# Optimization experiments

Measured on AMD Instinct MI355X. Metric: run time of the kernel, lower is better.

The kernel has to match this reference:

```python
import jax, jax.numpy as jnp
import numpy as np

B, L, H, NH, NB = 8, 200, 128, 4, 2
HD = H // NH
ITEM_NUM, TIME_SPAN = 50000, 256
PAD = -2.0**32 + 1.0


def setup_inputs() -> dict:
    key = jax.random.key(0)
    ks = jax.random.split(key, 32)
    def g(i, shape, s=0.02):
        return jax.random.normal(ks[i], shape, jnp.float32) * s
    item_emb = g(0, (ITEM_NUM + 1, H)).at[0].set(0.0)  # padding_idx=0
    return dict(
        user_ids=jax.random.randint(ks[1], (B,), 0, 1000),
        log_seqs=jax.random.randint(ks[2], (B, L), 0, ITEM_NUM),
        time_matrices=jax.random.randint(ks[3], (B, L, L), 0, TIME_SPAN + 1),
        pos_seqs=jax.random.randint(ks[4], (B, L), 0, ITEM_NUM + 1),
        neg_seqs=jax.random.randint(ks[5], (B, L), 0, ITEM_NUM + 1),
        item_emb=item_emb,
        pos_K_emb=g(6, (L, H)), pos_V_emb=g(7, (L, H)),
        time_K_emb=g(8, (TIME_SPAN + 1, H)), time_V_emb=g(9, (TIME_SPAN + 1, H)),
        attn_ln_g=jnp.ones((NB, H)), attn_ln_b=jnp.zeros((NB, H)),
        Wq=g(10, (NB, H, H)), bq=jnp.zeros((NB, H)),
        Wk=g(11, (NB, H, H)), bk=jnp.zeros((NB, H)),
        Wv=g(12, (NB, H, H)), bv=jnp.zeros((NB, H)),
        fwd_ln_g=jnp.ones((NB, H)), fwd_ln_b=jnp.zeros((NB, H)),
        W1=g(13, (NB, H, H)), b1=jnp.zeros((NB, H)),
        W2=g(14, (NB, H, H)), b2=jnp.zeros((NB, H)),
        last_ln_g=jnp.ones((H,)), last_ln_b=jnp.zeros((H,)),
    )


def _ln(x, g, b, eps=1e-8):
    m = x.mean(-1, keepdims=True)
    v = jnp.var(x, axis=-1, keepdims=True)
    return (x - m) / jnp.sqrt(v + eps) * g + b


def _heads(x):
    # [..., H] -> [NH, ..., HD]; matches torch.cat(torch.split(x, HD, -1), 0)
    y = x.reshape(x.shape[:-1] + (NH, HD))
    return jnp.moveaxis(y, -2, 0)


def reference(user_ids, log_seqs, time_matrices, pos_seqs, neg_seqs, item_emb,
              pos_K_emb, pos_V_emb, time_K_emb, time_V_emb,
              attn_ln_g, attn_ln_b, Wq, bq, Wk, bk, Wv, bv,
              fwd_ln_g, fwd_ln_b, W1, b1, W2, b2, last_ln_g, last_ln_b):
    # user_ids is unused in the original forward as well.
    tmask = log_seqs == 0                                  # [B,L] True = pad
    keep = (~tmask)[..., None].astype(jnp.float32)
    seqs = item_emb[log_seqs] * np.float32(np.sqrt(H))
    seqs = seqs * keep
    pKh = _heads(pos_K_emb)                                # [NH,L,HD]
    pVh = _heads(pos_V_emb)
    tKh = _heads(time_K_emb[time_matrices])                # [NH,B,L,L,HD]
    tVh = _heads(time_V_emb[time_matrices])
    causal = ~jnp.tril(jnp.ones((L, L), bool))             # True above diag -> masked
    bad = tmask[:, :, None] | causal[None]                 # [B,L,L]
    scale = np.float32(np.sqrt(HD))
    for i in range(NB):
        Qin = _ln(seqs, attn_ln_g[i], attn_ln_b[i])
        Qh = _heads(Qin @ Wq[i].T + bq[i])                 # [NH,B,L,HD]
        Kh = _heads(seqs @ Wk[i].T + bk[i])
        Vh = _heads(seqs @ Wv[i].T + bv[i])
        attn = (jnp.einsum('nbqd,nbkd->nbqk', Qh, Kh)
                + jnp.einsum('nbqd,nkd->nbqk', Qh, pKh)
                + jnp.einsum('nbqkd,nbqd->nbqk', tKh, Qh)) / scale
        attn = jnp.where(bad[None], PAD, attn)
        attn = jax.nn.softmax(attn, axis=-1)
        out = (jnp.einsum('nbqk,nbkd->nbqd', attn, Vh)
               + jnp.einsum('nbqk,nkd->nbqd', attn, pVh)
               + jnp.einsum('nbqk,nbqkd->nbqd', attn, tVh))
        out = jnp.moveaxis(out, 0, -2).reshape(seqs.shape)  # merge heads -> [B,L,H]
        seqs = Qin + out                                    # residual uses LN'd Q (as in source)
        seqs = _ln(seqs, fwd_ln_g[i], fwd_ln_b[i])
        ff = jax.nn.relu(seqs @ W1[i].T + b1[i]) @ W2[i].T + b2[i] + seqs
        seqs = ff * keep
    log_feats = _ln(seqs, last_ln_g, last_ln_b)
    pos_logits = (log_feats * item_emb[pos_seqs]).sum(-1)   # [B,L]
    neg_logits = (log_feats * item_emb[neg_seqs]).sum(-1)
    return pos_logits, neg_logits
```

## Files before the change

kernel.cpp:

```cpp
#include <hip/hip_runtime.h>

#define BB 8
#define LL 200
#define HH 128
#define NHEAD 4
#define HDIM 32
#define NBLK 2
#define BL (BB * LL)
#define NT 257
#define QT 8
#define NQT 25
#define SSP 208
#define KTP 66
#define TSP 132

static constexpr float SQRT_H    = 11.313708498984761f;
static constexpr float INV_SCALE = 0.17677669529663687f;
static constexpr float PADV      = -4294967295.0f;

__global__ void k_qkv_gemm(const float* __restrict__ seqs_in,
                           const int* __restrict__ log_seqs,
                           const float* __restrict__ item_emb,
                           const float* __restrict__ g, const float* __restrict__ bia,
                           const float* __restrict__ Wq, const float* __restrict__ bq,
                           const float* __restrict__ Wk, const float* __restrict__ bk,
                           const float* __restrict__ Wv, const float* __restrict__ bv,
                           const float* __restrict__ posK, const float* __restrict__ posV,
                           float* __restrict__ Qin, float* __restrict__ Q,
                           float* __restrict__ K, float* __restrict__ V) {
    int mt = blockIdx.x / 24, nt = blockIdx.x % 24;
    int matsel = nt >> 3;
    int jb = (nt & 7) * 16;
    int row0 = mt * 32;
    int tid = threadIdx.x;
    __shared__ float As[32 * TSP];
    __shared__ float Bs[16 * TSP];

    {
        int r = tid >> 3, seg = tid & 7;
        int row = row0 + r;
        float4 vv[4];
        if (seqs_in) {
            #pragma unroll
            for (int i = 0; i < 4; i++)
                vv[i] = *(const float4*)(seqs_in + (size_t)row * HH + seg * 16 + i * 4);
        } else {
            int idx = log_seqs[row];
            if (idx == 0) {
                #pragma unroll
                for (int i = 0; i < 4; i++) vv[i] = make_float4(0.f, 0.f, 0.f, 0.f);
            } else {
                #pragma unroll
                for (int i = 0; i < 4; i++) {
                    float4 e = *(const float4*)(item_emb + (size_t)idx * HH + seg * 16 + i * 4);
                    vv[i] = make_float4(e.x * SQRT_H, e.y * SQRT_H, e.z * SQRT_H, e.w * SQRT_H);
                }
            }
        }
        if (matsel == 0) {
            float s = 0.f, s2 = 0.f;
            #pragma unroll
            for (int i = 0; i < 4; i++) {
                s  += vv[i].x + vv[i].y + vv[i].z + vv[i].w;
                s2 += vv[i].x * vv[i].x + vv[i].y * vv[i].y + vv[i].z * vv[i].z + vv[i].w * vv[i].w;
            }
            #pragma unroll
            for (int off = 1; off < 8; off <<= 1) {
                s  += __shfl_xor(s, off);
                s2 += __shfl_xor(s2, off);
            }
            float mean = s * (1.f / HH);
            float var  = s2 * (1.f / HH) - mean * mean;
            float inv  = 1.f / sqrtf(var + 1e-8f);
            #pragma unroll
            for (int i = 0; i < 4; i++) {
                int k = seg * 16 + i * 4;
                float4 g4 = *(const float4*)(g + k);
                float4 b4 = *(const float4*)(bia + k);
                float4 y;
                y.x = (vv[i].x - mean) * inv * g4.x + b4.x;
                y.y = (vv[i].y - mean) * inv * g4.y + b4.y;
                y.z = (vv[i].z - mean) * inv * g4.z + b4.z;
                y.w = (vv[i].w - mean) * inv * g4.w + b4.w;
                *(float4*)&As[r * TSP + k] = y;
                if (nt == 0) *(float4*)(Qin + (size_t)row * HH + k) = y;
            }
        } else {
            #pragma unroll
            for (int i = 0; i < 4; i++)
                *(float4*)&As[r * TSP + seg * 16 + i * 4] = vv[i];
        }
    }
    {
        const float* W = (matsel == 0) ? Wq : (matsel == 1) ? Wk : Wv;
        int j = tid >> 4, seg = tid & 15;
        *(float4*)&Bs[j * TSP + seg * 8]     = *(const float4*)(W + (size_t)(jb + j) * HH + seg * 8);
        *(float4*)&Bs[j * TSP + seg * 8 + 4] = *(const float4*)(W + (size_t)(jb + j) * HH + seg * 8 + 4);
    }
    __syncthreads();

    int m = tid >> 3, jg = tid & 7;
    float acc0 = 0.f, acc1 = 0.f;
    const float* ar = &As[m * TSP];
    const float* b0r = &Bs[(jg * 2) * TSP];
    const float* b1r = &Bs[(jg * 2 + 1) * TSP];
    #pragma unroll 4
    for (int k4 = 0; k4 < 32; k4++) {
        float4 a = *(const float4*)(ar + k4 * 4);
        float4 b0 = *(const float4*)(b0r + k4 * 4);
        float4 b1 = *(const float4*)(b1r + k4 * 4);
        acc0 += a.x * b0.x + a.y * b0.y + a.z * b0.z + a.w * b0.w;
        acc1 += a.x * b1.x + a.y * b1.y + a.z * b1.z + a.w * b1.w;
    }
    int row = row0 + m;
    int col = jb + jg * 2;
    int l = row % LL;
    if (matsel == 0) {
        float2 bb = *(const float2*)(bq + col);
        *(float2*)(Q + (size_t)row * HH + col) =
            make_float2((acc0 + bb.x) * INV_SCALE, (acc1 + bb.y) * INV_SCALE);
    } else if (matsel == 1) {
        float2 bb = *(const float2*)(bk + col);
        float2 pk = *(const float2*)(posK + (size_t)l * HH + col);
        *(float2*)(K + (size_t)row * HH + col) =
            make_float2(acc0 + bb.x + pk.x, acc1 + bb.y + pk.y);
    } else {
        float2 bb = *(const float2*)(bv + col);
        float2 pv = *(const float2*)(posV + (size_t)l * HH + col);
        *(float2*)(V + (size_t)row * HH + col) =
            make_float2(acc0 + bb.x + pv.x, acc1 + bb.y + pv.y);
    }
}

__global__ void k_attn(const float* __restrict__ Q, const float* __restrict__ K,
                       const float* __restrict__ V,
                       const float* __restrict__ timeK, const float* __restrict__ timeV,
                       const int* __restrict__ tm,
                       float* __restrict__ att) {
    int bn = blockIdx.x & 31;
    int b = bn >> 2, n = bn & 3;
    int qt = (NQT - 1) - (blockIdx.x >> 5);
    int q0 = qt * QT;
    int kmax = q0 + QT - 1;
    int tid = threadIdx.x;
    int wv = tid >> 6, ln = tid & 63;

    __shared__ float Qs[QT * HDIM];
    __shared__ float KstT[2][HDIM * KTP];
    __shared__ float DTW[QT * NT];
    __shared__ float Ssc[QT * SSP];
    __shared__ unsigned short tmst[QT * LL];
    __shared__ float Ost[QT * HDIM];

    int nchS = (kmax >> 6) + 1;
    int ntot = 5 + nchS;

    auto stage = [&](int c, int buf) {
        const float* src;
        int base, lim;
        if (c < 5) { base = c * 64; src = timeK; lim = NT; }
        else       { base = (c - 5) * 64; src = K + ((size_t)(b * LL)) * HH; lim = LL; }
        #pragma unroll
        for (int pp = 0; pp < 2; pp++) {
            int idx = tid + pp * 256;
            int r = idx >> 3, d4 = idx & 7;
            int rr = base + r;
            float4 w = make_float4(0.f, 0.f, 0.f, 0.f);
            if (rr < lim) w = *(const float4*)(src + (size_t)rr * HH + n * HDIM + d4 * 4);
            KstT[buf][(d4 * 4 + 0) * KTP + r] = w.x;
            KstT[buf][(d4 * 4 + 1) * KTP + r] = w.y;
            KstT[buf][(d4 * 4 + 2) * KTP + r] = w.z;
            KstT[buf][(d4 * 4 + 3) * KTP + r] = w.w;
        }
    };

    Ost[tid] = 0.f;
    if (tid < 64) {
        int qi = tid >> 3, d4 = tid & 7;
        *(float4*)(Qs + qi * HDIM + d4 * 4) =
            *(const float4*)(Q + ((size_t)(b * LL + q0 + qi)) * HH + n * HDIM + d4 * 4);
    }
    #pragma unroll
    for (int qi = 0; qi < QT; qi++)
        if (tid < LL)
            tmst[qi * LL + tid] = (unsigned short)tm[((size_t)(b * LL + q0 + qi)) * LL + tid];
    stage(0, 0);
    __syncthreads();

    int k2 = tid & 31, qi_c = tid >> 5;

    for (int c = 0; c < ntot; c++) {
        int buf = c & 1;
        if (c + 1 < ntot) stage(c + 1, buf ^ 1);
        float a0 = 0.f, a1 = 0.f;
        #pragma unroll 4
        for (int d = 0; d < HDIM; d++) {
            float qv = Qs[qi_c * HDIM + d];
            float2 kv = *(const float2*)&KstT[buf][d * KTP + k2 * 2];
            a0 += qv * kv.x; a1 += qv * kv.y;
        }
        if (c < 5) {
            int tau0 = c * 64 + k2 * 2;
            if (tau0 < NT)     DTW[qi_c * NT + tau0]     = a0;
            if (tau0 + 1 < NT) DTW[qi_c * NT + tau0 + 1] = a1;
        } else {
            int q = q0 + qi_c;
            int k0 = (c - 5) * 64 + k2 * 2;
            if (k0 <= kmax)
                Ssc[qi_c * SSP + k0] = (k0 <= q) ? (a0 + DTW[qi_c * NT + tmst[qi_c * LL + k0]]) : PADV;
            if (k0 + 1 <= kmax)
                Ssc[qi_c * SSP + k0 + 1] = (k0 + 1 <= q) ? (a1 + DTW[qi_c * NT + tmst[qi_c * LL + k0 + 1]]) : PADV;
        }
        __syncthreads();
    }

    for (int idx = tid; idx < QT * NT; idx += 256) DTW[idx] = 0.f;
    __syncthreads();

    for (int rr = 0; rr < 2; rr++) {
        int qi = wv + rr * 4;
        int q = q0 + qi;
        float sv[4];
        float m = PADV;
        #pragma unroll
        for (int jj = 0; jj < 4; jj++) {
            int k = ln + 64 * jj;
            sv[jj] = (k <= q) ? Ssc[qi * SSP + k] : PADV;
            m = fmaxf(m, sv[jj]);
        }
        for (int off = 32; off; off >>= 1) m = fmaxf(m, __shfl_xor(m, off));
        float sum = 0.f;
        #pragma unroll
        for (int jj = 0; jj < 4; jj++) {
            int k = ln + 64 * jj;
            sv[jj] = (k <= q) ? __expf(sv[jj] - m) : 0.f;
            sum += sv[jj];
        }
        for (int off = 32; off; off >>= 1) sum += __shfl_xor(sum, off);
        float inv = 1.f / sum;
        #pragma unroll
        for (int jj = 0; jj < 4; jj++) {
            int k = ln + 64 * jj;
            float pr = sv[jj] * inv;
            if (k < SSP) Ssc[qi * SSP + k] = (k <= q) ? pr : 0.f;
            if (k <= q) atomicAdd(&DTW[qi * NT + tmst[qi * LL + k]], pr);
        }
    }
    __syncthreads();

    int d = tid & 31, kg = tid >> 5;
    float acc[QT] = {0,0,0,0,0,0,0,0};
    const float* vb = V + ((size_t)(b * LL)) * HH + n * HDIM + d;
    for (int k = kg; k <= kmax; k += 8) {
        float v = vb[(size_t)k * HH];
        #pragma unroll
        for (int qi = 0; qi < QT; qi++) acc[qi] += Ssc[qi * SSP + k] * v;
    }
    const float* tvb = timeV + n * HDIM + d;
    for (int t = kg; t < NT; t += 8) {
        float v = tvb[(size_t)t * HH];
        #pragma unroll
        for (int qi = 0; qi < QT; qi++) acc[qi] += DTW[qi * NT + t] * v;
    }
    #pragma unroll
    for (int qi = 0; qi < QT; qi++) atomicAdd(&Ost[qi * HDIM + d], acc[qi]);
    __syncthreads();
    {
        int qi = tid >> 5;
        att[((size_t)(b * LL + q0 + qi)) * HH + n * HDIM + (tid & 31)] = Ost[tid];
    }
}

__global__ void k_ff1(const float* __restrict__ Qin, const float* __restrict__ att,
                      const float* __restrict__ g, const float* __restrict__ bia,
                      const float* __restrict__ W1, const float* __restrict__ b1,
                      float* __restrict__ h1) {
    int mt = blockIdx.x >> 3, jb = (blockIdx.x & 7) * 16;
    int row0 = mt * 16;
    int tid = threadIdx.x;
    __shared__ float As[16 * TSP];
    __shared__ float Bs[16 * TSP];

    {
        int r = tid >> 4, seg = tid & 15;
        int row = row0 + r;
        float4 vv[2];
        #pragma unroll
        for (int i = 0; i < 2; i++) {
            int k = seg * 8 + i * 4;
            float4 q4 = *(const float4*)(Qin + (size_t)row * HH + k);
            float4 a4 = *(const float4*)(att + (size_t)row * HH + k);
            vv[i] = make_float4(q4.x + a4.x, q4.y + a4.y, q4.z + a4.z, q4.w + a4.w);
        }
        float s = 0.f, s2 = 0.f;
        #pragma unroll
        for (int i = 0; i < 2; i++) {
            s  += vv[i].x + vv[i].y + vv[i].z + vv[i].w;
            s2 += vv[i].x * vv[i].x + vv[i].y * vv[i].y + vv[i].z * vv[i].z + vv[i].w * vv[i].w;
        }
        #pragma unroll
        for (int off = 1; off < 16; off <<= 1) {
            s  += __shfl_xor(s, off);
            s2 += __shfl_xor(s2, off);
        }
        float mean = s * (1.f / HH);
        float var  = s2 * (1.f / HH) - mean * mean;
        float inv  = 1.f / sqrtf(var + 1e-8f);
        #pragma unroll
        for (int i = 0; i < 2; i++) {
            int k = seg * 8 + i * 4;
            float4 g4 = *(const float4*)(g + k);
            float4 b4 = *(const float4*)(bia + k);
            float4 y;
            y.x = (vv[i].x - mean) * inv * g4.x + b4.x;
            y.y = (vv[i].y - mean) * inv * g4.y + b4.y;
            y.z = (vv[i].z - mean) * inv * g4.z + b4.z;
            y.w = (vv[i].w - mean) * inv * g4.w + b4.w;
            *(float4*)&As[r * TSP + k] = y;
        }
    }
    {
        int j = tid >> 4, seg = tid & 15;
        *(float4*)&Bs[j * TSP + seg * 8]     = *(const float4*)(W1 + (size_t)(jb + j) * HH + seg * 8);
        *(float4*)&Bs[j * TSP + seg * 8 + 4] = *(const float4*)(W1 + (size_t)(jb + j) * HH + seg * 8 + 4);
    }
    __syncthreads();

    int m = tid >> 4, j = tid & 15;
    float acc = 0.f;
    const float* ar = &As[m * TSP];
    const float* br = &Bs[j * TSP];
    #pragma unroll 4
    for (int k4 = 0; k4 < 32; k4++) {
        float4 a = *(const float4*)(ar + k4 * 4);
        float4 b = *(const float4*)(br + k4 * 4);
        acc += a.x * b.x + a.y * b.y + a.z * b.z + a.w * b.w;
    }
    int col = jb + j;
    float t = acc + b1[col];
    h1[(size_t)(row0 + m) * HH + col] = t > 0.f ? t : 0.f;
}

__global__ void k_ff2(const float* __restrict__ h1,
                      const float* __restrict__ Qin, const float* __restrict__ att,
                      const float* __restrict__ g, const float* __restrict__ bia,
                      const float* __restrict__ W2, const float* __restrict__ b2,
                      const int* __restrict__ log_seqs,
                      float* __restrict__ out) {
    int mt = blockIdx.x >> 3, jb = (blockIdx.x & 7) * 16;
    int row0 = mt * 16;
    int tid = threadIdx.x;
    __shared__ float As[16 * TSP];
    __shared__ float Bs[16 * TSP];
    __shared__ float mu[16], rstd[16];

    {
        int r = tid >> 4, seg = tid & 15;
        int row = row0 + r;
        #pragma unroll
        for (int i = 0; i < 2; i++) {
            int k = seg * 8 + i * 4;
            *(float4*)&As[r * TSP + k] = *(const float4*)(h1 + (size_t)row * HH + k);
        }
        float s = 0.f, s2 = 0.f;
        #pragma unroll
        for (int i = 0; i < 2; i++) {
            int k = seg * 8 + i * 4;
            float4 q4 = *(const float4*)(Qin + (size_t)row * HH + k);
            float4 a4 = *(const float4*)(att + (size_t)row * HH + k);
            float4 v = make_float4(q4.x + a4.x, q4.y + a4.y, q4.z + a4.z, q4.w + a4.w);
            s  += v.x + v.y + v.z + v.w;
            s2 += v.x * v.x + v.y * v.y + v.z * v.z + v.w * v.w;
        }
        #pragma unroll
        for (int off = 1; off < 16; off <<= 1) {
            s  += __shfl_xor(s, off);
            s2 += __shfl_xor(s2, off);
        }
        float mean = s * (1.f / HH);
        float var  = s2 * (1.f / HH) - mean * mean;
        if (seg == 0) { mu[r] = mean; rstd[r] = 1.f / sqrtf(var + 1e-8f); }
    }
    {
        int j = tid >> 4, seg = tid & 15;
        *(float4*)&Bs[j * TSP + seg * 8]     = *(const float4*)(W2 + (size_t)(jb + j) * HH + seg * 8);
        *(float4*)&Bs[j * TSP + seg * 8 + 4] = *(const float4*)(W2 + (size_t)(jb + j) * HH + seg * 8 + 4);
    }
    __syncthreads();

    int m = tid >> 4, j = tid & 15;
    float acc = 0.f;
    const float* ar = &As[m * TSP];
    const float* br = &Bs[j * TSP];
    #pragma unroll 4
    for (int k4 = 0; k4 < 32; k4++) {
        float4 a = *(const float4*)(ar + k4 * 4);
        float4 b = *(const float4*)(br + k4 * 4);
        acc += a.x * b.x + a.y * b.y + a.z * b.z + a.w * b.w;
    }
    int row = row0 + m;
    int col = jb + j;
    float resid = Qin[(size_t)row * HH + col] + att[(size_t)row * HH + col];
    float y = (resid - mu[m]) * rstd[m] * g[col] + bia[col];
    float o = acc + b2[col] + y;
    if (log_seqs[row] == 0) o = 0.f;
    out[(size_t)row * HH + col] = o;
}

__global__ void k_lnlogits(const float* __restrict__ seqs,
                           const float* __restrict__ g, const float* __restrict__ bia,
                           const float* __restrict__ item_emb,
                           const int* __restrict__ pos, const int* __restrict__ neg,
                           float* __restrict__ out) {
    int row = blockIdx.x;
    int h = threadIdx.x;
    float v = seqs[(size_t)row * HH + h];
    float s = v, s2 = v * v;
    for (int off = 32; off; off >>= 1) {
        s  += __shfl_xor(s, off);
        s2 += __shfl_xor(s2, off);
    }
    __shared__ float r1[2], r2[2];
    if ((h & 63) == 0) { r1[h >> 6] = s; r2[h >> 6] = s2; }
    __syncthreads();
    float mean = (r1[0] + r1[1]) * (1.f / HH);
    float var  = (r2[0] + r2[1]) * (1.f / HH) - mean * mean;
    float inv = 1.f / sqrtf(var + 1e-8f);
    float f = (v - mean) * inv * g[h] + bia[h];

    int ip = pos[row], in_ = neg[row];
    float vp = f * item_emb[(size_t)ip * HH + h];
    float vn = f * item_emb[(size_t)in_ * HH + h];
    for (int off = 32; off; off >>= 1) {
        vp += __shfl_xor(vp, off);
        vn += __shfl_xor(vn, off);
    }
    __shared__ float rp[2], rn[2];
    if ((h & 63) == 0) { rp[h >> 6] = vp; rn[h >> 6] = vn; }
    __syncthreads();
    if (h == 0) {
        out[row]      = rp[0] + rp[1];
        out[BL + row] = rn[0] + rn[1];
    }
}

extern "C" void kernel_launch(void* const* d_in, const int* in_sizes, int n_in,
                              void* d_out, int out_size, void* d_ws, size_t ws_size,
                              hipStream_t stream) {
    const int* log_seqs   = (const int*)d_in[1];
    const int* tm         = (const int*)d_in[2];
    const int* pos_seqs   = (const int*)d_in[3];
    const int* neg_seqs   = (const int*)d_in[4];
    const float* item_emb = (const float*)d_in[5];
    const float* posK     = (const float*)d_in[6];
    const float* posV     = (const float*)d_in[7];
    const float* timeK    = (const float*)d_in[8];
    const float* timeV    = (const float*)d_in[9];
    const float* attn_g   = (const float*)d_in[10];
    const float* attn_b   = (const float*)d_in[11];
    const float* Wq       = (const float*)d_in[12];
    const float* bq       = (const float*)d_in[13];
    const float* Wk       = (const float*)d_in[14];
    const float* bk       = (const float*)d_in[15];
    const float* Wv       = (const float*)d_in[16];
    const float* bv       = (const float*)d_in[17];
    const float* fwd_g    = (const float*)d_in[18];
    const float* fwd_b    = (const float*)d_in[19];
    const float* W1       = (const float*)d_in[20];
    const float* b1       = (const float*)d_in[21];
    const float* W2       = (const float*)d_in[22];
    const float* b2       = (const float*)d_in[23];
    const float* last_g   = (const float*)d_in[24];
    const float* last_b   = (const float*)d_in[25];

    float* seqs = (float*)d_ws;
    float* Qin  = seqs + (size_t)BL * HH;
    float* Qb   = Qin  + (size_t)BL * HH;
    float* Kb   = Qb   + (size_t)BL * HH;
    float* Vb   = Kb   + (size_t)BL * HH;
    float* att  = Vb   + (size_t)BL * HH;
    float* h1   = att  + (size_t)BL * HH;

    for (int i = 0; i < NBLK; i++) {
        k_qkv_gemm<<<1200, 256, 0, stream>>>(i == 0 ? nullptr : seqs, log_seqs, item_emb,
                                             attn_g + i * HH, attn_b + i * HH,
                                             Wq + (size_t)i * HH * HH, bq + i * HH,
                                             Wk + (size_t)i * HH * HH, bk + i * HH,
                                             Wv + (size_t)i * HH * HH, bv + i * HH,
                                             posK, posV, Qin, Qb, Kb, Vb);
        k_attn<<<NQT * 32, 256, 0, stream>>>(Qb, Kb, Vb, timeK, timeV, tm, att);
        k_ff1<<<800, 256, 0, stream>>>(Qin, att, fwd_g + i * HH, fwd_b + i * HH,
                                       W1 + (size_t)i * HH * HH, b1 + i * HH, h1);
        k_ff2<<<800, 256, 0, stream>>>(h1, Qin, att, fwd_g + i * HH, fwd_b + i * HH,
                                       W2 + (size_t)i * HH * HH, b2 + i * HH,
                                       log_seqs, seqs);
    }
    k_lnlogits<<<BL, HH, 0, stream>>>(seqs, last_g, last_b, item_emb,
                                      pos_seqs, neg_seqs, (float*)d_out);
}
```

Baseline: 239.8 us.

## Fuse FFN layers and final LayerNorm logits into one kernel; cache Q in registers

The two feed-forward GEMM kernels and the final LayerNorm-plus-logits kernel become a single kernel. Each block handles 4 rows and keeps the LN output and the hidden activations in shared memory, so the h1 round trip through global memory and two launches per block go away. In the attention kernel the Q row is loaded into registers once, instead of being re-read from shared memory in every chunk. The trade-off is that each block now reloads both full 128x128 weight matrices into shared memory for only 4 rows, which adds weight traffic and leaves little compute per block to hide it.

```diff
diff --git a/kernel.cpp b/kernel.cpp
--- a/kernel.cpp
+++ b/kernel.cpp
@@ -13,6 +13,8 @@
 #define SSP 208
 #define KTP 66
 #define TSP 132
+#define BSP 66
+#define FSP 132
 
 static constexpr float SQRT_H    = 11.313708498984761f;
 static constexpr float INV_SCALE = 0.17677669529663687f;
@@ -189,15 +191,18 @@
 
     int k2 = tid & 31, qi_c = tid >> 5;
 
+    float qreg[HDIM];
+    #pragma unroll
+    for (int d = 0; d < HDIM; d++) qreg[d] = Qs[qi_c * HDIM + d];
+
     for (int c = 0; c < ntot; c++) {
         int buf = c & 1;
         if (c + 1 < ntot) stage(c + 1, buf ^ 1);
         float a0 = 0.f, a1 = 0.f;
-        #pragma unroll 4
+        #pragma unroll 8
         for (int d = 0; d < HDIM; d++) {
-            float qv = Qs[qi_c * HDIM + d];
             float2 kv = *(const float2*)&KstT[buf][d * KTP + k2 * 2];
-            a0 += qv * kv.x; a1 += qv * kv.y;
+            a0 += qreg[d] * kv.x; a1 += qreg[d] * kv.y;
         }
         if (c < 5) {
             int tau0 = c * 64 + k2 * 2;
@@ -271,176 +276,111 @@
     }
 }
 
-__global__ void k_ff1(const float* __restrict__ Qin, const float* __restrict__ att,
+__global__ void k_ffn(const float* __restrict__ Qin, const float* __restrict__ att,
                       const float* __restrict__ g, const float* __restrict__ bia,
                       const float* __restrict__ W1, const float* __restrict__ b1,
-                      float* __restrict__ h1) {
-    int mt = blockIdx.x >> 3, jb = (blockIdx.x & 7) * 16;
-    int row0 = mt * 16;
+                      const float* __restrict__ W2, const float* __restrict__ b2,
+                      const int* __restrict__ log_seqs,
+                      const float* __restrict__ lg, const float* __restrict__ lb,
+                      const float* __restrict__ item_emb,
+                      const int* __restrict__ pos, const int* __restrict__ neg,
+                      float* __restrict__ out, float* __restrict__ logits, int last) {
+    int row0 = blockIdx.x * 4;
     int tid = threadIdx.x;
-    __shared__ float As[16 * TSP];
-    __shared__ float Bs[16 * TSP];
+    int wv = tid >> 6, ln = tid & 63;
+    __shared__ float As[4 * FSP];
+    __shared__ float H1[4 * FSP];
+    __shared__ float Bs[128 * BSP];
 
     {
-        int r = tid >> 4, seg = tid & 15;
-        int row = row0 + r;
-        float4 vv[2];
-        #pragma unroll
-        for (int i = 0; i < 2; i++) {
-            int k = seg * 8 + i * 4;
-            float4 q4 = *(const float4*)(Qin + (size_t)row * HH + k);
-            float4 a4 = *(const float4*)(att + (size_t)row * HH + k);
-            vv[i] = make_float4(q4.x + a4.x, q4.y + a4.y, q4.z + a4.z, q4.w + a4.w);
-        }
-        float s = 0.f, s2 = 0.f;
-        #pragma unroll
-        for (int i = 0; i < 2; i++) {
-            s  += vv[i].x + vv[i].y + vv[i].z + vv[i].w;
-            s2 += vv[i].x * vv[i].x + vv[i].y * vv[i].y + vv[i].z * vv[i].z + vv[i].w * vv[i].w;
-        }
-        #pragma unroll
-        for (int off = 1; off < 16; off <<= 1) {
+        int row = row0 + wv;
+        float v0 = Qin[(size_t)row * HH + ln]      + att[(size_t)row * HH + ln];
+        float v1 = Qin[(size_t)row * HH + ln + 64] + att[(size_t)row * HH + ln + 64];
+        float s = v0 + v1, s2 = v0 * v0 + v1 * v1;
+        for (int off = 32; off; off >>= 1) {
             s  += __shfl_xor(s, off);
             s2 += __shfl_xor(s2, off);
         }
         float mean = s * (1.f / HH);
         float var  = s2 * (1.f / HH) - mean * mean;
         float inv  = 1.f / sqrtf(var + 1e-8f);
-        #pragma unroll
-        for (int i = 0; i < 2; i++) {
-            int k = seg * 8 + i * 4;
-            float4 g4 = *(const float4*)(g + k);
-            float4 b4 = *(const float4*)(bia + k);
-            float4 y;
-            y.x = (vv[i].x - mean) * inv * g4.x + b4.x;
-            y.y = (vv[i].y - mean) * inv * g4.y + b4.y;
-            y.z = (vv[i].z - mean) * inv * g4.z + b4.z;
-            y.w = (vv[i].w - mean) * inv * g4.w + b4.w;
-            *(float4*)&As[r * TSP + k] = y;
-        }
-    }
-    {
-        int j = tid >> 4, seg = tid & 15;
-        *(float4*)&Bs[j * TSP + seg * 8]     = *(const float4*)(W1 + (size_t)(jb + j) * HH + seg * 8);
-        *(float4*)&Bs[j * TSP + seg * 8 + 4] = *(const float4*)(W1 + (size_t)(jb + j) * HH + seg * 8 + 4);
-    }
-    __syncthreads();
-
-    int m = tid >> 4, j = tid & 15;
-    float acc = 0.f;
-    const float* ar = &As[m * TSP];
-    const float* br = &Bs[j * TSP];
-    #pragma unroll 4
-    for (int k4 = 0; k4 < 32; k4++) {
-        float4 a = *(const float4*)(ar + k4 * 4);
-        float4 b = *(const float4*)(br + k4 * 4);
-        acc += a.x * b.x + a.y * b.y + a.z * b.z + a.w * b.w;
-    }
-    int col = jb + j;
-    float t = acc + b1[col];
-    h1[(size_t)(row0 + m) * HH + col] = t > 0.f ? t : 0.f;
-}
-
-__global__ void k_ff2(const float* __restrict__ h1,
-                      const float* __restrict__ Qin, const float* __restrict__ att,
-                      const float* __restrict__ g, const float* __restrict__ bia,
-                      const float* __restrict__ W2, const float* __restrict__ b2,
-                      const int* __restrict__ log_seqs,
-                      float* __restrict__ out) {
-    int mt = blockIdx.x >> 3, jb = (blockIdx.x & 7) * 16;
-    int row0 = mt * 16;
-    int tid = threadIdx.x;
-    __shared__ float As[16 * TSP];
-    __shared__ float Bs[16 * TSP];
-    __shared__ float mu[16], rstd[16];
-
-    {
-        int r = tid >> 4, seg = tid & 15;
-        int row = row0 + r;
-        #pragma unroll
-        for (int i = 0; i < 2; i++) {
-            int k = seg * 8 + i * 4;
-            *(float4*)&As[r * TSP + k] = *(const float4*)(h1 + (size_t)row * HH + k);
-        }
-        float s = 0.f, s2 = 0.f;
-        #pragma unroll
-        for (int i = 0; i < 2; i++) {
-            int k = seg * 8 + i * 4;
-            float4 q4 = *(const float4*)(Qin + (size_t)row * HH + k);
-            float4 a4 = *(const float4*)(att + (size_t)row * HH + k);
-            float4 v = make_float4(q4.x + a4.x, q4.y + a4.y, q4.z + a4.z, q4.w + a4.w);
-            s  += v.x + v.y + v.z + v.w;
-            s2 += v.x * v.x + v.y * v.y + v.z * v.z + v.w * v.w;
-        }
-        #pragma unroll
-        for (int off = 1; off < 16; off <<= 1) {
+        As[wv * FSP + ln]      = (v0 - mean) * inv * g[ln]      + bia[ln];
+        As[wv * FSP + ln + 64] = (v1 - mean) * inv * g[ln + 64] + bia[ln + 64];
+    }
+    __syncthreads();
+
+    int jx = ln;
+    for (int c = 0; c < 2; c++) {
+        int k4 = tid & 31, jj0 = tid >> 5;
+        #pragma unroll
+        for (int p = 0; p < 8; p++) {
+            int jj = jj0 + p * 8;
+            float4 w = *(const float4*)(W1 + (size_t)(c * 64 + jj) * HH + k4 * 4);
+            Bs[(k4 * 4 + 0) * BSP + jj] = w.x;
+            Bs[(k4 * 4 + 1) * BSP + jj] = w.y;
+            Bs[(k4 * 4 + 2) * BSP + jj] = w.z;
+            Bs[(k4 * 4 + 3) * BSP + jj] = w.w;
+        }
+        __syncthreads();
+        float acc = 0.f;
+        #pragma unroll 8
+        for (int k = 0; k < HH; k++)
+            acc += As[wv * FSP + k] * Bs[k * BSP + jx];
+        int col = c * 64 + jx;
+        float t = acc + b1[col];
+        H1[wv * FSP + col] = t > 0.f ? t : 0.f;
+        __syncthreads();
+    }
+
+    int rowm = row0 + wv;
+    int keepz = (log_seqs[rowm] == 0);
+    for (int c = 0; c < 2; c++) {
+        int k4 = tid & 31, jj0 = tid >> 5;
+        #pragma unroll
+        for (int p = 0; p < 8; p++) {
+            int jj = jj0 + p * 8;
+            float4 w = *(const float4*)(W2 + (size_t)(c * 64 + jj) * HH + k4 * 4);
+            Bs[(k4 * 4 + 0) * BSP + jj] = w.x;
+            Bs[(k4 * 4 + 1) * BSP + jj] = w.y;
+            Bs[(k4 * 4 + 2) * BSP + jj] = w.z;
+            Bs[(k4 * 4 + 3) * BSP + jj] = w.w;
+        }
+        __syncthreads();
+        float acc = 0.f;
+        #pragma unroll 8
+        for (int k = 0; k < HH; k++)
+            acc += H1[wv * FSP + k] * Bs[k * BSP + jx];
+        int col = c * 64 + jx;
+        float o = acc + b2[col] + As[wv * FSP + col];
+        if (keepz) o = 0.f;
+        if (!last) out[(size_t)rowm * HH + col] = o;
+        As[wv * FSP + col] = o;
+        __syncthreads();
+    }
+
+    if (last) {
+        float o0 = As[wv * FSP + ln], o1 = As[wv * FSP + ln + 64];
+        float s = o0 + o1, s2 = o0 * o0 + o1 * o1;
+        for (int off = 32; off; off >>= 1) {
             s  += __shfl_xor(s, off);
             s2 += __shfl_xor(s2, off);
         }
         float mean = s * (1.f / HH);
         float var  = s2 * (1.f / HH) - mean * mean;
-        if (seg == 0) { mu[r] = mean; rstd[r] = 1.f / sqrtf(var + 1e-8f); }
-    }
-    {
-        int j = tid >> 4, seg = tid & 15;
-        *(float4*)&Bs[j * TSP + seg * 8]     = *(const float4*)(W2 + (size_t)(jb + j) * HH + seg * 8);
-        *(float4*)&Bs[j * TSP + seg * 8 + 4] = *(const float4*)(W2 + (size_t)(jb + j) * HH + seg * 8 + 4);
-    }
-    __syncthreads();
-
-    int m = tid >> 4, j = tid & 15;
-    float acc = 0.f;
-    const float* ar = &As[m * TSP];
-    const float* br = &Bs[j * TSP];
-    #pragma unroll 4
-    for (int k4 = 0; k4 < 32; k4++) {
-        float4 a = *(const float4*)(ar + k4 * 4);
-        float4 b = *(const float4*)(br + k4 * 4);
-        acc += a.x * b.x + a.y * b.y + a.z * b.z + a.w * b.w;
-    }
-    int row = row0 + m;
-    int col = jb + j;
-    float resid = Qin[(size_t)row * HH + col] + att[(size_t)row * HH + col];
-    float y = (resid - mu[m]) * rstd[m] * g[col] + bia[col];
-    float o = acc + b2[col] + y;
-    if (log_seqs[row] == 0) o = 0.f;
-    out[(size_t)row * HH + col] = o;
-}
-
-__global__ void k_lnlogits(const float* __restrict__ seqs,
-                           const float* __restrict__ g, const float* __restrict__ bia,
-                           const float* __restrict__ item_emb,
-                           const int* __restrict__ pos, const int* __restrict__ neg,
-                           float* __restrict__ out) {
-    int row = blockIdx.x;
-    int h = threadIdx.x;
-    float v = seqs[(size_t)row * HH + h];
-    float s = v, s2 = v * v;
-    for (int off = 32; off; off >>= 1) {
-        s  += __shfl_xor(s, off);
-        s2 += __shfl_xor(s2, off);
-    }
-    __shared__ float r1[2], r2[2];
-    if ((h & 63) == 0) { r1[h >> 6] = s; r2[h >> 6] = s2; }
-    __syncthreads();
-    float mean = (r1[0] + r1[1]) * (1.f / HH);
-    float var  = (r2[0] + r2[1]) * (1.f / HH) - mean * mean;
-    float inv = 1.f / sqrtf(var + 1e-8f);
-    float f = (v - mean) * inv * g[h] + bia[h];
-
-    int ip = pos[row], in_ = neg[row];
-    float vp = f * item_emb[(size_t)ip * HH + h];
-    float vn = f * item_emb[(size_t)in_ * HH + h];
-    for (int off = 32; off; off >>= 1) {
-        vp += __shfl_xor(vp, off);
-        vn += __shfl_xor(vn, off);
-    }
-    __shared__ float rp[2], rn[2];
-    if ((h & 63) == 0) { rp[h >> 6] = vp; rn[h >> 6] = vn; }
-    __syncthreads();
-    if (h == 0) {
-        out[row]      = rp[0] + rp[1];
-        out[BL + row] = rn[0] + rn[1];
+        float inv  = 1.f / sqrtf(var + 1e-8f);
+        float f0 = (o0 - mean) * inv * lg[ln]      + lb[ln];
+        float f1 = (o1 - mean) * inv * lg[ln + 64] + lb[ln + 64];
+        int ip = pos[rowm], in_ = neg[rowm];
+        float vp = f0 * item_emb[(size_t)ip * HH + ln] + f1 * item_emb[(size_t)ip * HH + ln + 64];
+        float vn = f0 * item_emb[(size_t)in_ * HH + ln] + f1 * item_emb[(size_t)in_ * HH + ln + 64];
+        for (int off = 32; off; off >>= 1) {
+            vp += __shfl_xor(vp, off);
+            vn += __shfl_xor(vn, off);
+        }
+        if (ln == 0) {
+            logits[rowm]      = vp;
+            logits[BL + rowm] = vn;
+        }
     }
 }
 
@@ -479,7 +419,6 @@
     float* Kb   = Qb   + (size_t)BL * HH;
     float* Vb   = Kb   + (size_t)BL * HH;
     float* att  = Vb   + (size_t)BL * HH;
-    float* h1   = att  + (size_t)BL * HH;
 
     for (int i = 0; i < NBLK; i++) {
         k_qkv_gemm<<<1200, 256, 0, stream>>>(i == 0 ? nullptr : seqs, log_seqs, item_emb,
@@ -489,12 +428,11 @@
                                              Wv + (size_t)i * HH * HH, bv + i * HH,
                                              posK, posV, Qin, Qb, Kb, Vb);
         k_attn<<<NQT * 32, 256, 0, stream>>>(Qb, Kb, Vb, timeK, timeV, tm, att);
-        k_ff1<<<800, 256, 0, stream>>>(Qin, att, fwd_g + i * HH, fwd_b + i * HH,
-                                       W1 + (size_t)i * HH * HH, b1 + i * HH, h1);
-        k_ff2<<<800, 256, 0, stream>>>(h1, Qin, att, fwd_g + i * HH, fwd_b + i * HH,
-                                       W2 + (size_t)i * HH * HH, b2 + i * HH,
-                                       log_seqs, seqs);
-    }
-    k_lnlogits<<<BL, HH, 0, stream>>>(seqs, last_g, last_b, item_emb,
-                                      pos_seqs, neg_seqs, (float*)d_out);
+        k_ffn<<<BL / 4, 256, 0, stream>>>(Qin, att, fwd_g + i * HH, fwd_b + i * HH,
+                                          W1 + (size_t)i * HH * HH, b1 + i * HH,
+                                          W2 + (size_t)i * HH * HH, b2 + i * HH,
+                                          log_seqs, last_g, last_b, item_emb,
+                                          pos_seqs, neg_seqs,
+                                          seqs, (float*)d_out, (i == NBLK - 1) ? 1 : 0);
+    }
 }
```

After: 251.6 us. 4.9% more time.
